# Kernel optimization log

Measured on AMD Instinct MI355X. Metric: run time of the kernel, lower is better.

Reference implementation:

```python
import jax, jax.numpy as jnp
from jax import lax
import numpy as np

UNITS = 256
H = W = 64
INPUT_DIM = 128
FLAT = 64 * (H - 3) * (W - 3)  # conv stack output after same-conv, valid-conv, 2x2 avgpool stride 1


def setup_inputs() -> dict:
    key = jax.random.key(0)
    ks = jax.random.split(key, 8)
    s = lambda k, shape, fan: jax.random.normal(k, shape, jnp.float32) / np.sqrt(fan)
    return {
        "inputs": jax.random.normal(ks[0], (1, INPUT_DIM), jnp.float32),
        "memory": jax.random.normal(ks[1], (H * W, UNITS), jnp.float32),
        "conv_kernel1": s(ks[2], (3, 3, UNITS, 32), 9 * UNITS),
        "conv_kernel2": s(ks[3], (3, 3, 32, 64), 9 * 32),
        "conv_dense1": s(ks[4], (FLAT, 128), FLAT),
        "conv_dense2": s(ks[5], (128, UNITS), 128),
        "context_kernel": s(ks[6], (INPUT_DIM + UNITS, UNITS), INPUT_DIM + UNITS),
        "recurr_kernel": s(ks[7], (INPUT_DIM + UNITS, UNITS), UNITS),
        "x": 32,
        "y": 17,
    }


def reference(inputs, memory, conv_kernel1, conv_kernel2, conv_dense1,
              conv_dense2, context_kernel, recurrent_kernel=None, recurr_kernel=None,
              x=32, y=17):
    rec = recurr_kernel if recurr_kernel is not None else recurrent_kernel
    input_dim = inputs.shape[-1]
    # memory: (H*W, units) -> (1, units, H, W)  (channels_first)
    mem = memory.T.reshape(1, UNITS, H, W)
    dn = ("NCHW", "HWIO", "NCHW")
    c1 = lax.conv_general_dilated(mem, conv_kernel1, (1, 1), "SAME", dimension_numbers=dn)   # (1,32,H,W)
    c2 = lax.conv_general_dilated(c1, conv_kernel2, (1, 1), "VALID", dimension_numbers=dn)   # (1,64,H-2,W-2)
    pool = lax.reduce_window(c2, 0.0, lax.add, (1, 1, 2, 2), (1, 1, 1, 1), "VALID") * 0.25   # (1,64,H-3,W-3)
    flat = pool.reshape(1, -1)
    r_t = (flat @ conv_dense1) @ conv_dense2                      # (1, units)
    q_t = jnp.concatenate([inputs, r_t], axis=-1) @ context_kernel  # (1, units)
    m = mem[0]                                                    # (units, H, W)
    m2 = m.reshape(UNITS, H * W)
    scores = q_t @ m2                                             # (1, H*W)
    at = jax.nn.softmax(scores, axis=-1)                          # softmax over all positions
    c_t = at @ m2.T                                               # (1, units) attention read
    write_kernel = rec[:input_dim]
    write_update = rec[input_dim:]
    s_t = inputs @ write_kernel                                   # (1, units)
    global_imp = jnp.sum(s_t * r_t)
    local_imp = jnp.sum(s_t * c_t)
    mem_t = m[:, x, y][None, :]                                   # gather single slot (1, units)
    mem_t = mem_t + local_imp / (local_imp + global_imp) * ((mem_t - s_t) @ write_update)
    new_mem = m.at[:, x, y].set(mem_t[0])                         # scatter slot back
    return c_t, r_t, new_mem
```

## Files before the change

### kernel.cpp

```cpp
#include <hip/hip_runtime.h>

#define FLAT  238144
#define NB_R1 931

#define W_C2   0
#define W_P1   246016
#define W_RT   365184
#define W_ST   365440
#define W_QT   365696
#define W_SC   365952
#define W_STAT 370048
#define W_PC   370176
#define W_WARM 386560
#define W_END  386576

#define F_C2   140416
#define F_P1   386432
#define F_RT   505600
#define F_ST   505856
#define F_QT   506112
#define F_SC   506368
#define F_STAT 510464
#define F_PC   510592

__device__ __forceinline__ int read_idx(const int* p) {
    unsigned int u = (unsigned int)*p;
    int ex = (int)((u >> 23) & 0xFF);
    int v;
    if (ex >= 118 && ex <= 140) {
        union { unsigned int i; float f; } c; c.i = u;
        v = (int)(c.f + 0.5f);
    } else {
        v = (int)u;
    }
    return v < 0 ? 0 : (v > 63 ? 63 : v);
}

__global__ __launch_bounds__(256) void k_conv1(const float* __restrict__ mem,
                                               const float* __restrict__ k1,
                                               float* __restrict__ c1p) {
    __shared__ float sm[32 * 105];
    __shared__ __align__(16) float sk[9 * 32 * 32];
    int t = threadIdx.x;
    int th = (blockIdx.x >> 3) * 8;
    int tw = (blockIdx.x & 7) * 8;
    int chunk = blockIdx.y;
    for (int u = t; u < 800; u += 256) {
        int pix = u >> 3;
        int c4 = u & 7;
        int hh = th - 1 + pix / 10;
        int ww = tw - 1 + pix % 10;
        float4 v = make_float4(0.f, 0.f, 0.f, 0.f);
        if ((unsigned)hh < 64u && (unsigned)ww < 64u)
            v = *(const float4*)(mem + (size_t)(hh * 64 + ww) * 256
                                     + chunk * 32 + c4 * 4);
        int ib = c4 * 4;
        sm[(ib    ) * 105 + pix] = v.x;
        sm[(ib + 1) * 105 + pix] = v.y;
        sm[(ib + 2) * 105 + pix] = v.z;
        sm[(ib + 3) * 105 + pix] = v.w;
    }
    for (int u = t; u < 2304; u += 256) {
        int tap = u >> 8;
        int r   = u & 255;
        const float4* src = (const float4*)(k1 + (size_t)tap * 8192
                                               + (size_t)chunk * 1024);
        *(float4*)&sk[tap * 1024 + r * 4] = src[r];
    }
    __syncthreads();
    int lh = (t & 63) >> 3, lw = t & 7, og = t >> 6;
    float acc[8];
    #pragma unroll
    for (int j = 0; j < 8; ++j) acc[j] = 0.f;
    for (int dh = 0; dh < 3; ++dh)
        for (int dw = 0; dw < 3; ++dw) {
            int pixb = (lh + dh) * 10 + (lw + dw);
            const float* kt = sk + (dh * 3 + dw) * 1024 + og * 8;
            #pragma unroll 4
            for (int i = 0; i < 32; ++i) {
                float m = sm[i * 105 + pixb];
                float4 ka = *(const float4*)(kt + i * 32);
                float4 kb = *(const float4*)(kt + i * 32 + 4);
                acc[0] += m * ka.x; acc[1] += m * ka.y;
                acc[2] += m * ka.z; acc[3] += m * ka.w;
                acc[4] += m * kb.x; acc[5] += m * kb.y;
                acc[6] += m * kb.z; acc[7] += m * kb.w;
            }
        }
    int p = (th + lh) * 64 + tw + lw;
    float* dst = c1p + (size_t)chunk * 131072 + (size_t)(og * 8) * 4096 + p;
    #pragma unroll
    for (int j = 0; j < 8; ++j)
        dst[(size_t)j * 4096] = acc[j];
}

__global__ __launch_bounds__(256) void k_c1red(float* __restrict__ c1p) {
    int idx = blockIdx.x * 256 + threadIdx.x;
    float s = 0.f;
    #pragma unroll
    for (int c = 0; c < 8; ++c) s += c1p[(size_t)c * 131072 + idx];
    c1p[idx] = s;
}

__global__ __launch_bounds__(256) void k_conv2(const float* __restrict__ c1p,
                                               const float* __restrict__ k2,
                                               float* __restrict__ c2,
                                               int nchunks) {
    __shared__ float sm[32 * 104];
    __shared__ __align__(16) float sk2[9 * 32 * 16];
    int t = threadIdx.x;
    int th = (blockIdx.x >> 3) * 8;
    int tw = (blockIdx.x & 7) * 8;
    int o0 = blockIdx.y * 16;
    for (int u = t; u < 3200; u += 256) {
        int i = u / 100;
        int pix = u % 100;
        int hh = th + pix / 10;
        int ww = tw + pix % 10;
        float v = 0.f;
        if (hh < 64 && ww < 64) {
            const float* p = c1p + (size_t)i * 4096 + hh * 64 + ww;
            for (int c = 0; c < nchunks; ++c)
                v += p[(size_t)c * 131072];
        }
        sm[i * 104 + pix] = v;
    }
    for (int u = t; u < 1152; u += 256) {
        int tap = u >> 7;
        int r = u & 127;
        int i = r >> 2, o4 = r & 3;
        *(float4*)&sk2[tap * 512 + i * 16 + o4 * 4] =
            *(const float4*)(k2 + (size_t)tap * 2048 + i * 64 + o0 + o4 * 4);
    }
    __syncthreads();
    int pix = t & 63;
    int lh = pix >> 3, lw = pix & 7, og = t >> 6;
    float acc[4] = {0.f, 0.f, 0.f, 0.f};
    for (int dh = 0; dh < 3; ++dh)
        for (int dw = 0; dw < 3; ++dw) {
            int pixb = (lh + dh) * 10 + (lw + dw);
            const float* kt = sk2 + (dh * 3 + dw) * 512 + og * 4;
            #pragma unroll 8
            for (int i = 0; i < 32; ++i) {
                float m = sm[i * 104 + pixb];
                float4 kv = *(const float4*)(kt + i * 16);
                acc[0] += m * kv.x; acc[1] += m * kv.y;
                acc[2] += m * kv.z; acc[3] += m * kv.w;
            }
        }
    int h = th + lh, w = tw + lw;
    if (h < 62 && w < 62) {
        #pragma unroll
        for (int j = 0; j < 4; ++j)
            c2[(size_t)(o0 + og * 4 + j) * 3844 + h * 62 + w] = acc[j];
    }
}

__global__ __launch_bounds__(256) void k_r1pt(const float* __restrict__ c2,
                                              const float* __restrict__ d1,
                                              float* __restrict__ p1,
                                              const float* __restrict__ mem,
                                              const int* __restrict__ px,
                                              const int* __restrict__ py,
                                              float* __restrict__ outm,
                                              const float* __restrict__ d2,
                                              const float* __restrict__ ck,
                                              const float* __restrict__ rec,
                                              float* __restrict__ warm,
                                              int withx) {
    __shared__ __align__(16) float SM[4160];
    int t = threadIdx.x;
    int bid = blockIdx.x;
    int fb = -1;
    if (!withx) {
        fb = bid;
    } else if (bid < 256) {
        int tu = bid;
        float* tile = SM;
        int p0 = (tu & 63) * 64;
        int u0 = (tu >> 6) * 64;
        int x = read_idx(px), y = read_idx(py);
        int pxy = x * 64 + y;
        int lane = t & 63, grp = t >> 6;
        for (int r = 0; r < 16; ++r) {
            int pr = grp + r * 4;
            tile[pr * 65 + lane] = mem[(size_t)(p0 + pr) * 256 + u0 + lane];
        }
        __syncthreads();
        for (int r = 0; r < 16; ++r) {
            int ur = grp + r * 4;
            if (p0 + lane != pxy)
                outm[(size_t)(u0 + ur) * 4096 + p0 + lane] = tile[lane * 65 + ur];
        }
        return;
    } else if (bid < 256 + NB_R1) {
        fb = bid - 256;
    } else {
        int wu = bid - (256 + NB_R1);
        float a = 0.f;
        for (int k = 0; k < 14; ++k) {
            int j = (wu * 256 + t) + k * 4096;
            float4 v;
            if (j < 8192)        v = ((const float4*)d2 )[j];
            else if (j < 32768)  v = ((const float4*)rec)[j - 8192];
            else                 v = ((const float4*)ck )[j - 32768];
            a += v.x + v.y + v.z + v.w;
        }
        SM[t] = a;
        __syncthreads();
        if (t == 0) {
            float s = 0.f;
            for (int i = 0; i < 256; ++i) s += SM[i];
            warm[wu] = s;
        }
        return;
    }
    {
        float* pl   = SM;
        float* sred = SM + 256;
        int f0 = fb * 256;
        int fmax = FLAT - f0; if (fmax > 256) fmax = 256;
        for (int s = t; s < fmax; s += 256) {
            int f = f0 + s;
            int o = f / 3721;
            int r = f % 3721;
            int h = r / 61, w = r % 61;
            const float* b = c2 + (size_t)o * 3844 + h * 62 + w;
            pl[s] = 0.25f * (b[0] + b[1] + b[62] + b[63]);
        }
        __syncthreads();
        int jq = t & 31, g = t >> 5;
        float4 a = make_float4(0.f, 0.f, 0.f, 0.f);
        if (fmax == 256) {
            #pragma unroll 8
            for (int it = 0; it < 32; ++it) {
                int s = g + it * 8;
                float m = pl[s];
                float4 dv = *(const float4*)(d1 + (size_t)(f0 + s) * 128 + jq * 4);
                a.x += m * dv.x; a.y += m * dv.y; a.z += m * dv.z; a.w += m * dv.w;
            }
        } else {
            for (int s = g; s < fmax; s += 8) {
                float m = pl[s];
                float4 dv = *(const float4*)(d1 + (size_t)(f0 + s) * 128 + jq * 4);
                a.x += m * dv.x; a.y += m * dv.y; a.z += m * dv.z; a.w += m * dv.w;
            }
        }
        *(float4*)&sred[(g * 32 + jq) * 4] = a;
        __syncthreads();
        if (t < 32) {
            float4 s4 = make_float4(0.f, 0.f, 0.f, 0.f);
            #pragma unroll
            for (int gg = 0; gg < 8; ++gg) {
                float4 v = *(const float4*)&sred[(gg * 32 + t) * 4];
                s4.x += v.x; s4.y += v.y; s4.z += v.z; s4.w += v.w;
            }
            *(float4*)(p1 + (size_t)fb * 128 + t * 4) = s4;
        }
    }
}

__global__ __launch_bounds__(1024) void k_fused(const float* __restrict__ p1,
                                                const float* __restrict__ d2,
                                                const float* __restrict__ inp,
                                                const float* __restrict__ ck,
                                                const float* __restrict__ rec,
                                                float* __restrict__ rt,
                                                float* __restrict__ qt,
                                                float* __restrict__ st) {
    __shared__ float p2s[8][128];
    __shared__ float s_r1[128], s_in[128], s_rt[256];
    int t = threadIdx.x;
    int j = t & 127, part = t >> 7;
    int b0 = part * 117;
    int b1 = b0 + 117; if (b1 > NB_R1) b1 = NB_R1;
    float s = 0.f;
    #pragma unroll 4
    for (int b = b0; b < b1; ++b) s += p1[b * 128 + j];
    p2s[part][j] = s;
    if (t < 128) s_in[t] = inp[t];
    __syncthreads();
    if (t < 128) {
        float r = 0.f;
        #pragma unroll
        for (int c = 0; c < 8; ++c) r += p2s[c][t];
        s_r1[t] = r;
    }
    __syncthreads();
    if (t < 256) {
        float a = 0.f;
        #pragma unroll 8
        for (int k = 0; k < 128; ++k) a += s_r1[k] * d2[k * 256 + t];
        rt[t] = a; s_rt[t] = a;
        float sv = 0.f;
        #pragma unroll 8
        for (int k = 0; k < 128; ++k) sv += s_in[k] * rec[k * 256 + t];
        st[t] = sv;
    }
    __syncthreads();
    if (t < 256) {
        float q = 0.f;
        #pragma unroll 8
        for (int k = 0; k < 128; ++k) q += s_in[k] * ck[k * 256 + t];
        #pragma unroll 8
        for (int k = 0; k < 256; ++k) q += s_rt[k] * ck[(128 + k) * 256 + t];
        qt[t] = q;
    }
}

__global__ __launch_bounds__(256) void k_scores(const float* __restrict__ qt,
                                                const float* __restrict__ mem,
                                                float* __restrict__ sc,
                                                float* __restrict__ stat) {
    __shared__ float q[256];
    __shared__ float rowv[64];
    int t = threadIdx.x;
    int bid = blockIdx.x;
    q[t] = qt[t];
    __syncthreads();
    int wave = t >> 6, lane = t & 63;
    float qx = q[lane * 4], qy = q[lane * 4 + 1],
          qz = q[lane * 4 + 2], qw = q[lane * 4 + 3];
    for (int r = 0; r < 16; ++r) {
        int p = bid * 64 + wave * 16 + r;
        float4 m = *(const float4*)(mem + (size_t)p * 256 + lane * 4);
        float acc = m.x * qx + m.y * qy + m.z * qz + m.w * qw;
        for (int off = 32; off; off >>= 1) acc += __shfl_down(acc, off);
        if (lane == 0) rowv[wave * 16 + r] = acc;
    }
    __syncthreads();
    if (t < 64) sc[bid * 64 + t] = rowv[t];
    if (t == 0) {
        float mb = rowv[0];
        for (int i = 1; i < 64; ++i) mb = fmaxf(mb, rowv[i]);
        float sb = 0.f;
        for (int i = 0; i < 64; ++i) sb += expf(rowv[i] - mb);
        stat[bid * 2]     = mb;
        stat[bid * 2 + 1] = sb;
    }
}

__global__ __launch_bounds__(256) void k_ctp(const float* __restrict__ stat,
                                             const float* __restrict__ sc,
                                             const float* __restrict__ mem,
                                             float* __restrict__ pc) {
    __shared__ float sm_[64], ss_[64], aux[2], aL[64];
    int t = threadIdx.x;
    int bid = blockIdx.x;
    if (t < 64) { sm_[t] = stat[t * 2]; ss_[t] = stat[t * 2 + 1]; }
    __syncthreads();
    if (t == 0) {
        float M = sm_[0];
        for (int i = 1; i < 64; ++i) M = fmaxf(M, sm_[i]);
        float S = 0.f;
        for (int i = 0; i < 64; ++i) S += ss_[i] * expf(sm_[i] - M);
        aux[0] = M; aux[1] = 1.f / S;
    }
    __syncthreads();
    float M = aux[0], invS = aux[1];
    int p0 = bid * 64;
    if (t < 64) aL[t] = expf(sc[p0 + t] - M) * invS;
    __syncthreads();
    float acc = 0.f;
    #pragma unroll 8
    for (int pp = 0; pp < 64; ++pp)
        acc += aL[pp] * mem[(size_t)(p0 + pp) * 256 + t];
    pc[bid * 256 + t] = acc;
}

__global__ __launch_bounds__(256) void k_final(const float* __restrict__ rt,
                                               const float* __restrict__ st,
                                               const float* __restrict__ pc,
                                               const float* __restrict__ mem,
                                               const float* __restrict__ rec,
                                               const int* __restrict__ px,
                                               const int* __restrict__ py,
                                               float* __restrict__ out) {
    __shared__ float s_diff[256], red[256];
    int t = threadIdx.x;
    int x = read_idx(px), y = read_idx(py);
    int pxy = x * 64 + y;
    float ctv = 0.f;
    #pragma unroll 8
    for (int b = 0; b < 64; ++b) ctv += pc[b * 256 + t];
    float stv = st[t], rtv = rt[t];
    float memt = mem[(size_t)pxy * 256 + t];
    red[t] = stv * rtv; __syncthreads();
    for (int s = 128; s; s >>= 1) { if (t < s) red[t] += red[t + s]; __syncthreads(); }
    float gimp = red[0]; __syncthreads();
    red[t] = stv * ctv; __syncthreads();
    for (int s = 128; s; s >>= 1) { if (t < s) red[t] += red[t + s]; __syncthreads(); }
    float limp = red[0];
    s_diff[t] = memt - stv;
    __syncthreads();
    float d = 0.f;
    #pragma unroll 8
    for (int k = 0; k < 256; ++k)
        d += s_diff[k] * rec[(128 + k) * 256 + t];
    float frac = limp / (limp + gimp);
    out[t] = ctv;
    out[256 + t] = rtv;
    out[512 + (size_t)t * 4096 + pxy] = memt + frac * d;
}

__global__ __launch_bounds__(256) void k_transpose(const float* __restrict__ mem,
                                                   const int* __restrict__ px,
                                                   const int* __restrict__ py,
                                                   float* __restrict__ outm) {
    __shared__ float tile[64][65];
    int t = threadIdx.x;
    int p0 = blockIdx.x * 64;
    int u0 = blockIdx.y * 64;
    int x = read_idx(px), y = read_idx(py);
    int pxy = x * 64 + y;
    int lane = t & 63, grp = t >> 6;
    for (int r = 0; r < 16; ++r) {
        int pr = grp + r * 4;
        tile[pr][lane] = mem[(size_t)(p0 + pr) * 256 + u0 + lane];
    }
    __syncthreads();
    for (int r = 0; r < 16; ++r) {
        int ur = grp + r * 4;
        if (p0 + lane != pxy)
            outm[(size_t)(u0 + ur) * 4096 + p0 + lane] = tile[lane][ur];
    }
}

extern "C" void kernel_launch(void* const* d_in, const int* in_sizes, int n_in,
                              void* d_out, int out_size, void* d_ws, size_t ws_size,
                              hipStream_t stream) {
    const float* inp = (const float*)d_in[0];
    const float* mem = (const float*)d_in[1];
    const float* k1  = (const float*)d_in[2];
    const float* k2  = (const float*)d_in[3];
    const float* d1  = (const float*)d_in[4];
    const float* d2  = (const float*)d_in[5];
    const float* ck  = (const float*)d_in[6];
    const float* rec = (const float*)d_in[7];
    const int* px = (const int*)d_in[8];
    const int* py = (const int*)d_in[9];
    float* out = (float*)d_out;
    float* scr = out + 512;
    float* ws  = (float*)d_ws;

    bool useWs = (ws != nullptr) && (ws_size >= (size_t)W_END * sizeof(float));

    if (useWs) {
        k_conv1<<<dim3(64, 8), 256, 0, stream>>>(mem, k1, scr);
        k_conv2<<<dim3(64, 4), 256, 0, stream>>>(scr, k2, ws + W_C2, 8);
        k_r1pt<<<256 + NB_R1 + 16, 256, 0, stream>>>(ws + W_C2, d1, ws + W_P1,
                                                     mem, px, py, scr,
                                                     d2, ck, rec,
                                                     ws + W_WARM, 1);
        k_fused<<<1, 1024, 0, stream>>>(ws + W_P1, d2, inp, ck, rec,
                                        ws + W_RT, ws + W_QT, ws + W_ST);
        k_scores<<<64, 256, 0, stream>>>(ws + W_QT, mem, ws + W_SC,
                                         ws + W_STAT);
        k_ctp<<<64, 256, 0, stream>>>(ws + W_STAT, ws + W_SC, mem, ws + W_PC);
        k_final<<<1, 256, 0, stream>>>(ws + W_RT, ws + W_ST, ws + W_PC,
                                       mem, rec, px, py, out);
    } else {
        k_conv1<<<dim3(64, 8), 256, 0, stream>>>(mem, k1, scr);
        k_c1red<<<512, 256, 0, stream>>>(scr);
        k_conv2<<<dim3(64, 4), 256, 0, stream>>>(scr, k2, scr + F_C2, 1);
        k_r1pt<<<NB_R1, 256, 0, stream>>>(scr + F_C2, d1, scr + F_P1,
                                          mem, px, py, scr,
                                          d2, ck, rec, scr + F_PC + 16384, 0);
        k_fused<<<1, 1024, 0, stream>>>(scr + F_P1, d2, inp, ck, rec,
                                        scr + F_RT, scr + F_QT, scr + F_ST);
        k_scores<<<64, 256, 0, stream>>>(scr + F_QT, mem, scr + F_SC,
                                         scr + F_STAT);
        k_ctp<<<64, 256, 0, stream>>>(scr + F_STAT, scr + F_SC, mem,
                                      scr + F_PC);
        k_final<<<1, 256, 0, stream>>>(scr + F_RT, scr + F_ST, scr + F_PC,
                                       mem, rec, px, py, out);
        k_transpose<<<dim3(64, 4), 256, 0, stream>>>(mem, px, py, out + 512);
    }
}
```

Measured before the change: 326.1 us.

## Fuse softmax-weighted context into scores kernel and precompute input projections early

```diff
diff --git a/kernel.cpp b/kernel.cpp
--- a/kernel.cpp
+++ b/kernel.cpp
@@ -8,18 +8,18 @@
 #define W_RT   365184
 #define W_ST   365440
 #define W_QT   365696
-#define W_SC   365952
-#define W_STAT 370048
-#define W_PC   370176
-#define W_WARM 386560
-#define W_END  386576
+#define W_QTA  365952
+#define W_STAT 366208
+#define W_PC   366336
+#define W_WARM 382720
+#define W_END  382736
 
 #define F_C2   140416
 #define F_P1   386432
 #define F_RT   505600
 #define F_ST   505856
 #define F_QT   506112
-#define F_SC   506368
+#define F_QTA  506368
 #define F_STAT 510464
 #define F_PC   510592
 
@@ -166,6 +166,9 @@
                                               const float* __restrict__ d2,
                                               const float* __restrict__ ck,
                                               const float* __restrict__ rec,
+                                              const float* __restrict__ inp,
+                                              float* __restrict__ st,
+                                              float* __restrict__ qta,
                                               float* __restrict__ warm,
                                               int withx) {
     __shared__ __align__(16) float SM[4160];
@@ -195,16 +198,30 @@
         return;
     } else if (bid < 256 + NB_R1) {
         fb = bid - 256;
+    } else if (bid == 256 + NB_R1) {
+        float sv = 0.f;
+        #pragma unroll 8
+        for (int k = 0; k < 128; ++k) sv += inp[k] * rec[k * 256 + t];
+        st[t] = sv;
+        return;
+    } else if (bid == 257 + NB_R1) {
+        float q = 0.f;
+        #pragma unroll 8
+        for (int k = 0; k < 128; ++k) q += inp[k] * ck[k * 256 + t];
+        qta[t] = q;
+        return;
     } else {
-        int wu = bid - (256 + NB_R1);
+        int wu = bid - (258 + NB_R1);
         float a = 0.f;
-        for (int k = 0; k < 14; ++k) {
-            int j = (wu * 256 + t) + k * 4096;
-            float4 v;
-            if (j < 8192)        v = ((const float4*)d2 )[j];
-            else if (j < 32768)  v = ((const float4*)rec)[j - 8192];
-            else                 v = ((const float4*)ck )[j - 32768];
-            a += v.x + v.y + v.z + v.w;
+        for (int k = 0; k < 12; ++k) {
+            int j = (wu * 256 + t) + k * 3584;
+            if (j < 40960) {
+                float4 v;
+                if (j < 8192)        v = ((const float4*)d2 )[j];
+                else if (j < 24576)  v = ((const float4*)rec)[j];
+                else                 v = ((const float4*)ck )[j - 16384];
+                a += v.x + v.y + v.z + v.w;
+            }
         }
         SM[t] = a;
         __syncthreads();
@@ -265,9 +282,11 @@
                                                 const float* __restrict__ inp,
                                                 const float* __restrict__ ck,
                                                 const float* __restrict__ rec,
+                                                const float* __restrict__ qta,
                                                 float* __restrict__ rt,
                                                 float* __restrict__ qt,
-                                                float* __restrict__ st) {
+                                                float* __restrict__ st,
+                                                int haveAux) {
     __shared__ float p2s[8][128];
     __shared__ float s_r1[128], s_in[128], s_rt[256];
     int t = threadIdx.x;
@@ -292,16 +311,23 @@
         #pragma unroll 8
         for (int k = 0; k < 128; ++k) a += s_r1[k] * d2[k * 256 + t];
         rt[t] = a; s_rt[t] = a;
-        float sv = 0.f;
-        #pragma unroll 8
-        for (int k = 0; k < 128; ++k) sv += s_in[k] * rec[k * 256 + t];
-        st[t] = sv;
+        if (!haveAux) {
+            float sv = 0.f;
+            #pragma unroll 8
+            for (int k = 0; k < 128; ++k) sv += s_in[k] * rec[k * 256 + t];
+            st[t] = sv;
+        }
     }
     __syncthreads();
     if (t < 256) {
-        float q = 0.f;
-        #pragma unroll 8
-        for (int k = 0; k < 128; ++k) q += s_in[k] * ck[k * 256 + t];
+        float q;
+        if (haveAux) {
+            q = qta[t];
+        } else {
+            q = 0.f;
+            #pragma unroll 8
+            for (int k = 0; k < 128; ++k) q += s_in[k] * ck[k * 256 + t];
+        }
         #pragma unroll 8
         for (int k = 0; k < 256; ++k) q += s_rt[k] * ck[(128 + k) * 256 + t];
         qt[t] = q;
@@ -310,10 +336,11 @@
 
 __global__ __launch_bounds__(256) void k_scores(const float* __restrict__ qt,
                                                 const float* __restrict__ mem,
-                                                float* __restrict__ sc,
-                                                float* __restrict__ stat) {
+                                                float* __restrict__ stat,
+                                                float* __restrict__ pc) {
     __shared__ float q[256];
-    __shared__ float rowv[64];
+    __shared__ float rowv[64], aL[64];
+    __shared__ float mbS;
     int t = threadIdx.x;
     int bid = blockIdx.x;
     q[t] = qt[t];
@@ -321,46 +348,29 @@
     int wave = t >> 6, lane = t & 63;
     float qx = q[lane * 4], qy = q[lane * 4 + 1],
           qz = q[lane * 4 + 2], qw = q[lane * 4 + 3];
+    int p0 = bid * 64;
     for (int r = 0; r < 16; ++r) {
-        int p = bid * 64 + wave * 16 + r;
+        int p = p0 + wave * 16 + r;
         float4 m = *(const float4*)(mem + (size_t)p * 256 + lane * 4);
         float acc = m.x * qx + m.y * qy + m.z * qz + m.w * qw;
         for (int off = 32; off; off >>= 1) acc += __shfl_down(acc, off);
         if (lane == 0) rowv[wave * 16 + r] = acc;
     }
     __syncthreads();
-    if (t < 64) sc[bid * 64 + t] = rowv[t];
     if (t == 0) {
         float mb = rowv[0];
         for (int i = 1; i < 64; ++i) mb = fmaxf(mb, rowv[i]);
+        mbS = mb;
+    }
+    __syncthreads();
+    if (t < 64) aL[t] = expf(rowv[t] - mbS);
+    __syncthreads();
+    if (t == 0) {
         float sb = 0.f;
-        for (int i = 0; i < 64; ++i) sb += expf(rowv[i] - mb);
-        stat[bid * 2]     = mb;
+        for (int i = 0; i < 64; ++i) sb += aL[i];
+        stat[bid * 2]     = mbS;
         stat[bid * 2 + 1] = sb;
     }
-}
-
-__global__ __launch_bounds__(256) void k_ctp(const float* __restrict__ stat,
-                                             const float* __restrict__ sc,
-                                             const float* __restrict__ mem,
-                                             float* __restrict__ pc) {
-    __shared__ float sm_[64], ss_[64], aux[2], aL[64];
-    int t = threadIdx.x;
-    int bid = blockIdx.x;
-    if (t < 64) { sm_[t] = stat[t * 2]; ss_[t] = stat[t * 2 + 1]; }
-    __syncthreads();
-    if (t == 0) {
-        float M = sm_[0];
-        for (int i = 1; i < 64; ++i) M = fmaxf(M, sm_[i]);
-        float S = 0.f;
-        for (int i = 0; i < 64; ++i) S += ss_[i] * expf(sm_[i] - M);
-        aux[0] = M; aux[1] = 1.f / S;
-    }
-    __syncthreads();
-    float M = aux[0], invS = aux[1];
-    int p0 = bid * 64;
-    if (t < 64) aL[t] = expf(sc[p0 + t] - M) * invS;
-    __syncthreads();
     float acc = 0.f;
     #pragma unroll 8
     for (int pp = 0; pp < 64; ++pp)
@@ -370,6 +380,7 @@
 
 __global__ __launch_bounds__(256) void k_final(const float* __restrict__ rt,
                                                const float* __restrict__ st,
+                                               const float* __restrict__ stat,
                                                const float* __restrict__ pc,
                                                const float* __restrict__ mem,
                                                const float* __restrict__ rec,
@@ -377,12 +388,25 @@
                                                const int* __restrict__ py,
                                                float* __restrict__ out) {
     __shared__ float s_diff[256], red[256];
+    __shared__ float sm_[64], wb[64], aux[2];
     int t = threadIdx.x;
     int x = read_idx(px), y = read_idx(py);
     int pxy = x * 64 + y;
+    if (t < 64) sm_[t] = stat[t * 2];
+    __syncthreads();
+    if (t == 0) {
+        float M = sm_[0];
+        for (int i = 1; i < 64; ++i) M = fmaxf(M, sm_[i]);
+        float S = 0.f;
+        for (int i = 0; i < 64; ++i) S += stat[i * 2 + 1] * expf(sm_[i] - M);
+        aux[0] = M; aux[1] = 1.f / S;
+    }
+    __syncthreads();
+    if (t < 64) wb[t] = expf(sm_[t] - aux[0]) * aux[1];
+    __syncthreads();
     float ctv = 0.f;
     #pragma unroll 8
-    for (int b = 0; b < 64; ++b) ctv += pc[b * 256 + t];
+    for (int b = 0; b < 64; ++b) ctv += pc[b * 256 + t] * wb[b];
     float stv = st[t], rtv = rt[t];
     float memt = mem[(size_t)pxy * 256 + t];
     red[t] = stv * rtv; __syncthreads();
@@ -448,32 +472,30 @@
     if (useWs) {
         k_conv1<<<dim3(64, 8), 256, 0, stream>>>(mem, k1, scr);
         k_conv2<<<dim3(64, 4), 256, 0, stream>>>(scr, k2, ws + W_C2, 8);
-        k_r1pt<<<256 + NB_R1 + 16, 256, 0, stream>>>(ws + W_C2, d1, ws + W_P1,
-                                                     mem, px, py, scr,
-                                                     d2, ck, rec,
-                                                     ws + W_WARM, 1);
+        k_r1pt<<<256 + NB_R1 + 16, 256, 0, stream>>>(
+            ws + W_C2, d1, ws + W_P1, mem, px, py, scr,
+            d2, ck, rec, inp, ws + W_ST, ws + W_QTA, ws + W_WARM, 1);
         k_fused<<<1, 1024, 0, stream>>>(ws + W_P1, d2, inp, ck, rec,
-                                        ws + W_RT, ws + W_QT, ws + W_ST);
-        k_scores<<<64, 256, 0, stream>>>(ws + W_QT, mem, ws + W_SC,
-                                         ws + W_STAT);
-        k_ctp<<<64, 256, 0, stream>>>(ws + W_STAT, ws + W_SC, mem, ws + W_PC);
-        k_final<<<1, 256, 0, stream>>>(ws + W_RT, ws + W_ST, ws + W_PC,
-                                       mem, rec, px, py, out);
+                                        ws + W_QTA, ws + W_RT, ws + W_QT,
+                                        ws + W_ST, 1);
+        k_scores<<<64, 256, 0, stream>>>(ws + W_QT, mem, ws + W_STAT,
+                                         ws + W_PC);
+        k_final<<<1, 256, 0, stream>>>(ws + W_RT, ws + W_ST, ws + W_STAT,
+                                       ws + W_PC, mem, rec, px, py, out);
     } else {
         k_conv1<<<dim3(64, 8), 256, 0, stream>>>(mem, k1, scr);
         k_c1red<<<512, 256, 0, stream>>>(scr);
         k_conv2<<<dim3(64, 4), 256, 0, stream>>>(scr, k2, scr + F_C2, 1);
-        k_r1pt<<<NB_R1, 256, 0, stream>>>(scr + F_C2, d1, scr + F_P1,
-                                          mem, px, py, scr,
-                                          d2, ck, rec, scr + F_PC + 16384, 0);
+        k_r1pt<<<NB_R1, 256, 0, stream>>>(
+            scr + F_C2, d1, scr + F_P1, mem, px, py, scr,
+            d2, ck, rec, inp, scr + F_ST, scr + F_QTA, scr + F_PC + 16384, 0);
         k_fused<<<1, 1024, 0, stream>>>(scr + F_P1, d2, inp, ck, rec,
-                                        scr + F_RT, scr + F_QT, scr + F_ST);
-        k_scores<<<64, 256, 0, stream>>>(scr + F_QT, mem, scr + F_SC,
-                                         scr + F_STAT);
-        k_ctp<<<64, 256, 0, stream>>>(scr + F_STAT, scr + F_SC, mem,
-                                      scr + F_PC);
-        k_final<<<1, 256, 0, stream>>>(scr + F_RT, scr + F_ST, scr + F_PC,
-                                       mem, rec, px, py, out);
+                                        scr + F_QTA, scr + F_RT, scr + F_QT,
+                                        scr + F_ST, 0);
+        k_scores<<<64, 256, 0, stream>>>(scr + F_QT, mem, scr + F_STAT,
+                                         scr + F_PC);
+        k_final<<<1, 256, 0, stream>>>(scr + F_RT, scr + F_ST, scr + F_STAT,
+                                       scr + F_PC, mem, rec, px, py, out);
         k_transpose<<<dim3(64, 4), 256, 0, stream>>>(mem, px, py, out + 512);
     }
 }
```

Result: faster. 314.6 us (-3.5%).
